# Kernel optimization log

Hardware: AMD Instinct MI355X
Metric: run time of the kernel (lower is better)

Reference implementation:

```python
import jax, jax.numpy as jnp
import numpy as np

D_MODEL = 768
D_STATE = 16
D_CONV = 4
EXPAND = 2
D_INNER = EXPAND * D_MODEL  # 1536
DT_RANK = -(-D_MODEL // 16)  # ceil(768/16) = 48
BATCH = 1
SEQ = 2048


def _silu(v):
    return v * jax.nn.sigmoid(v)


def setup_inputs() -> dict:
    key = jax.random.key(0)
    ks = jax.random.split(key, 8)
    s = 0.02
    x = jax.random.normal(ks[0], (BATCH, SEQ, D_MODEL), jnp.float32)
    in_proj_w = jax.random.normal(ks[1], (2 * D_INNER, D_MODEL), jnp.float32) * s
    conv_w = jax.random.normal(ks[2], (D_INNER, 1, D_CONV), jnp.float32) * s  # depthwise, groups=D_INNER
    conv_b = jnp.zeros((D_INNER,), jnp.float32)
    x_proj_w = jax.random.normal(ks[3], (DT_RANK + 2 * D_STATE, D_INNER), jnp.float32) * s
    dt_proj_w = jax.random.normal(ks[4], (D_INNER, DT_RANK), jnp.float32) * s
    dt_proj_b = jax.random.normal(ks[5], (D_INNER,), jnp.float32) * 0.01
    # A = repeat_interleave(arange(1, d_state+1), d_inner rows); A_log = log(A)
    A_log = jnp.log(jnp.tile(jnp.arange(1, D_STATE + 1, dtype=jnp.float32)[None, :], (D_INNER, 1)))
    D = jnp.ones((D_INNER,), jnp.float32)
    out_proj_w = jax.random.normal(ks[6], (D_MODEL, D_INNER), jnp.float32) * s
    return {"x": x, "in_proj_w": in_proj_w, "conv_w": conv_w, "conv_b": conv_b,
            "x_proj_w": x_proj_w, "dt_proj_w": dt_proj_w, "dt_proj_b": dt_proj_b,
            "A_log": A_log, "D": D, "out_proj_w": out_proj_w}


def reference(x, in_proj_w, conv_w, conv_b, x_proj_w, dt_proj_w, dt_proj_b, A_log, D, out_proj_w):
    b, L, d = x.shape
    # in_proj then split into x-branch and gate z
    xz = x @ in_proj_w.T                       # (b, L, 2*d_inner)
    xh, z = jnp.split(xz, 2, axis=-1)          # each (b, L, d_inner)
    # causal depthwise conv1d: torch pads d_conv-1 both sides then slices [:L];
    # equivalent to left-pad d_conv-1, right-pad 0
    xc = jnp.transpose(xh, (0, 2, 1))          # (b, d_inner, L)
    xc = jax.lax.conv_general_dilated(
        xc, conv_w, window_strides=(1,), padding=[(D_CONV - 1, 0)],
        feature_group_count=D_INNER, dimension_numbers=("NCH", "OIH", "NCH"))
    xc = xc + conv_b[None, :, None]
    u = _silu(jnp.transpose(xc, (0, 2, 1)))    # (b, L, d_inner)
    # input-dependent dt, B, C
    x_dbl = u @ x_proj_w.T                     # (b, L, dt_rank + 2*d_state)
    dt, Bm, Cm = jnp.split(x_dbl, [DT_RANK, DT_RANK + D_STATE], axis=-1)
    dt = jax.nn.softplus(dt @ dt_proj_w.T + dt_proj_b)  # (b, L, d_inner)
    A = -jnp.exp(A_log)                        # (d_inner, d_state)
    # selective scan via cumprod/cumsum (faithful to source math)
    dA = jnp.exp(dt[..., None] * A[None, None])              # (b, L, d_inner, d_state)
    dBu = dt[..., None] * Bm[:, :, None, :] * u[..., None]   # (b, L, d_inner, d_state)
    p = jnp.cumprod(dA, axis=1)
    eps = jnp.finfo(u.dtype).eps
    p_safe = jnp.maximum(p, eps)
    g = jnp.cumsum(dBu / p_safe, axis=1)
    h = g * p
    y = jnp.sum(h * Cm[:, :, None, :], axis=-1) + D * u      # (b, L, d_inner)
    y = y * _silu(z)
    return y @ out_proj_w.T                    # (b, L, d_model); dropout=identity (eval)
```

## Files before the change

### kernel.cpp

```cpp
#include <hip/hip_runtime.h>
#include <hip/hip_bf16.h>

#define LSEQ 2048
#define DMODEL 768
#define DINNER 1536
#define DSTATE 16
#define DTRANK 48
#define XDBL_W (DTRANK + 2*DSTATE)
#define CHUNK 64
#define NCHUNK (LSEQ / CHUNK)
#define NDN (DINNER * DSTATE)
#define FEPS 1.1920928955078125e-07f
#define SPLITK 8
#define OSPLIT 4
#define LDST 68

typedef short bf16x8 __attribute__((ext_vector_type(8)));
typedef float f32x4 __attribute__((ext_vector_type(4)));
typedef unsigned short u16;

__device__ __forceinline__ u16 f2bf_rn(float f) {
    unsigned u = __float_as_uint(f);
    unsigned r = u + 0x7FFFu + ((u >> 16) & 1u);
    return (u16)(r >> 16);
}
__device__ __forceinline__ float bf2f(u16 h) {
    return __uint_as_float(((unsigned)h) << 16);
}

__global__ __launch_bounds__(256) void cvt_split(
    const float* __restrict__ src, u16* __restrict__ hi, u16* __restrict__ lo, int n)
{
    int i = (blockIdx.x * 256 + threadIdx.x) * 4;
    if (i >= n) return;
    float4 v = *(const float4*)&src[i];
    u16 h0 = f2bf_rn(v.x), h1 = f2bf_rn(v.y), h2 = f2bf_rn(v.z), h3 = f2bf_rn(v.w);
    u16 l0 = f2bf_rn(v.x - bf2f(h0));
    u16 l1 = f2bf_rn(v.y - bf2f(h1));
    u16 l2 = f2bf_rn(v.z - bf2f(h2));
    u16 l3 = f2bf_rn(v.w - bf2f(h3));
    ushort4 hv = make_ushort4(h0, h1, h2, h3);
    ushort4 lv = make_ushort4(l0, l1, l2, l3);
    *(ushort4*)&hi[i] = hv;
    *(ushort4*)&lo[i] = lv;
}

__global__ __launch_bounds__(256) void mfma_gemm_tn(
    const u16* __restrict__ Ahi, const u16* __restrict__ Alo,
    const u16* __restrict__ Bhi, const u16* __restrict__ Blo,
    float* __restrict__ C, int ldc, int ldk, int Klen)
{
    __shared__ u16 lds[2 * 4 * 4096];
    const int tid = threadIdx.x;
    const int wid = tid >> 6;
    const int lane = tid & 63;
    const int m0 = blockIdx.x * 128;
    const int n0 = blockIdx.y * 128;
    const int Koff = blockIdx.z * Klen;

    const int st_subrow = lane >> 2;
    const int st_cphys = lane & 3;
    const u16* myplane = (wid == 0) ? Ahi : (wid == 1) ? Alo : (wid == 2) ? Bhi : Blo;
    const int rowbase = (wid < 2) ? m0 : n0;

    f32x4 acc[4][4] = {};
    const int wm = (wid >> 1) * 64;
    const int wn = (wid & 1) * 64;
    const int fr = lane & 15;
    const int fc = lane >> 4;
    const int nsteps = Klen / 32;

    auto stage = [&](int buf, int k0) {
#pragma unroll
        for (int j = 0; j < 8; ++j) {
            int row = j * 16 + st_subrow;
            int clog = st_cphys ^ ((row >> 1) & 3);
            const u16* g = myplane + (size_t)(rowbase + row) * ldk + k0 + clog * 8;
            u16* l = &lds[buf * 16384 + wid * 4096 + j * 512];
            __builtin_amdgcn_global_load_lds(
                (const __attribute__((address_space(1))) unsigned int*)g,
                (__attribute__((address_space(3))) unsigned int*)l, 16, 0, 0);
        }
    };

    stage(0, Koff);
    int cur = 0;
    for (int t = 0; t < nsteps; ++t) {
        __syncthreads();
        if (t + 1 < nsteps) stage(cur ^ 1, Koff + (t + 1) * 32);

        bf16x8 ah[4], al[4], bh[4], bl[4];
        const bf16x8* L = (const bf16x8*)&lds[cur * 16384];
#pragma unroll
        for (int mi = 0; mi < 4; ++mi) {
            int r = wm + mi * 16 + fr;
            int idx = r * 4 + (fc ^ ((r >> 1) & 3));
            ah[mi] = L[idx];
            al[mi] = L[512 + idx];
        }
#pragma unroll
        for (int nj = 0; nj < 4; ++nj) {
            int r = wn + nj * 16 + fr;
            int idx = r * 4 + (fc ^ ((r >> 1) & 3));
            bh[nj] = L[1024 + idx];
            bl[nj] = L[1536 + idx];
        }
#pragma unroll
        for (int mi = 0; mi < 4; ++mi)
#pragma unroll
            for (int nj = 0; nj < 4; ++nj) {
                acc[mi][nj] = __builtin_amdgcn_mfma_f32_16x16x32_bf16(ah[mi], bh[nj], acc[mi][nj], 0, 0, 0);
                acc[mi][nj] = __builtin_amdgcn_mfma_f32_16x16x32_bf16(ah[mi], bl[nj], acc[mi][nj], 0, 0, 0);
                acc[mi][nj] = __builtin_amdgcn_mfma_f32_16x16x32_bf16(al[mi], bh[nj], acc[mi][nj], 0, 0, 0);
            }
        cur ^= 1;
    }

    float* Cz = C + (size_t)blockIdx.z * LSEQ * ldc;
#pragma unroll
    for (int mi = 0; mi < 4; ++mi) {
        int row_b = m0 + wm + mi * 16 + (lane >> 4) * 4;
#pragma unroll
        for (int nj = 0; nj < 4; ++nj) {
            int col = n0 + wn + nj * 16 + (lane & 15);
#pragma unroll
            for (int r = 0; r < 4; ++r)
                Cz[(size_t)(row_b + r) * ldc + col] = acc[mi][nj][r];
        }
    }
}

__global__ __launch_bounds__(256) void reduce4(
    const float* __restrict__ Ppart, float* __restrict__ out, int n)
{
    int i = (blockIdx.x * 256 + threadIdx.x) * 4;
    if (i >= n) return;
    float4 a0 = *(const float4*)&Ppart[i];
    float4 a1 = *(const float4*)&Ppart[(size_t)n + i];
    float4 a2 = *(const float4*)&Ppart[(size_t)2 * n + i];
    float4 a3 = *(const float4*)&Ppart[(size_t)3 * n + i];
    float4 r;
    r.x = ((a0.x + a1.x) + a2.x) + a3.x;
    r.y = ((a0.y + a1.y) + a2.y) + a3.y;
    r.z = ((a0.z + a1.z) + a2.z) + a3.z;
    r.w = ((a0.w + a1.w) + a2.w) + a3.w;
    *(float4*)&out[i] = r;
}

template<int EPI>
__global__ __launch_bounds__(256) void gemm_tn(
    const float* __restrict__ A, int lda,
    const float* __restrict__ B, int ldb,
    float* __restrict__ C, int ldc,
    int M, int N, int K,
    const float* __restrict__ bias)
{
    __shared__ float As[16][64 + 4];
    __shared__ float Bs[16][64 + 4];
    const int tid = threadIdx.x;
    const int m0 = blockIdx.x * 64;
    const int n0 = blockIdx.y * 64;
    const int tx = tid & 15;
    const int ty = tid >> 4;
    const int lr = tid >> 4;
    const int lc = tid & 15;
    float acc[4][4] = {};

    for (int k0 = 0; k0 < K; k0 += 16) {
        const int k = k0 + lc;
#pragma unroll
        for (int i = 0; i < 4; ++i) {
            int m = m0 + lr + i * 16;
            As[lc][lr + i * 16] = (m < M) ? A[(size_t)m * lda + k] : 0.f;
        }
#pragma unroll
        for (int i = 0; i < 4; ++i) {
            int n = n0 + lr + i * 16;
            Bs[lc][lr + i * 16] = (n < N) ? B[(size_t)n * ldb + k] : 0.f;
        }
        __syncthreads();
#pragma unroll
        for (int kk = 0; kk < 16; ++kk) {
            float a[4], b[4];
#pragma unroll
            for (int i = 0; i < 4; ++i) a[i] = As[kk][ty * 4 + i];
#pragma unroll
            for (int j = 0; j < 4; ++j) b[j] = Bs[kk][tx * 4 + j];
#pragma unroll
            for (int i = 0; i < 4; ++i)
#pragma unroll
                for (int j = 0; j < 4; ++j)
                    acc[i][j] = fmaf(a[i], b[j], acc[i][j]);
        }
        __syncthreads();
    }

#pragma unroll
    for (int i = 0; i < 4; ++i) {
        int m = m0 + ty * 4 + i;
        if (m >= M) continue;
#pragma unroll
        for (int j = 0; j < 4; ++j) {
            int n = n0 + tx * 4 + j;
            if (n >= N) continue;
            float v = acc[i][j];
            if (EPI == 1) {
                v += bias[n];
                v = fmaxf(v, 0.f) + log1pf(expf(-fabsf(v)));
            }
            C[(size_t)m * ldc + n] = v;
        }
    }
}

__global__ __launch_bounds__(256) void gemm_tn_splitk(
    const float* __restrict__ A, int lda,
    const float* __restrict__ B, int ldb,
    float* __restrict__ Cpart, int ldc,
    int M, int N, int Kchunk)
{
    __shared__ float As[16][64 + 4];
    __shared__ float Bs[16][64 + 4];
    const int tid = threadIdx.x;
    const int m0 = blockIdx.x * 64;
    const int n0 = blockIdx.y * 64;
    const int kb = blockIdx.z * Kchunk;
    const int tx = tid & 15;
    const int ty = tid >> 4;
    const int lr = tid >> 4;
    const int lc = tid & 15;
    float acc[4][4] = {};

    for (int k0 = kb; k0 < kb + Kchunk; k0 += 16) {
        const int k = k0 + lc;
#pragma unroll
        for (int i = 0; i < 4; ++i) {
            int m = m0 + lr + i * 16;
            As[lc][lr + i * 16] = (m < M) ? A[(size_t)m * lda + k] : 0.f;
        }
#pragma unroll
        for (int i = 0; i < 4; ++i) {
            int n = n0 + lr + i * 16;
            Bs[lc][lr + i * 16] = (n < N) ? B[(size_t)n * ldb + k] : 0.f;
        }
        __syncthreads();
#pragma unroll
        for (int kk = 0; kk < 16; ++kk) {
            float a[4], b[4];
#pragma unroll
            for (int i = 0; i < 4; ++i) a[i] = As[kk][ty * 4 + i];
#pragma unroll
            for (int j = 0; j < 4; ++j) b[j] = Bs[kk][tx * 4 + j];
#pragma unroll
            for (int i = 0; i < 4; ++i)
#pragma unroll
                for (int j = 0; j < 4; ++j)
                    acc[i][j] = fmaf(a[i], b[j], acc[i][j]);
        }
        __syncthreads();
    }

    float* Cs = Cpart + (size_t)blockIdx.z * M * ldc;
#pragma unroll
    for (int i = 0; i < 4; ++i) {
        int m = m0 + ty * 4 + i;
        if (m >= M) continue;
#pragma unroll
        for (int j = 0; j < 4; ++j) {
            int n = n0 + tx * 4 + j;
            if (n >= N) continue;
            Cs[(size_t)m * ldc + n] = acc[i][j];
        }
    }
}

__global__ __launch_bounds__(256) void splitk_reduce(
    const float* __restrict__ Ppart, float* __restrict__ out, int n)
{
    int i = blockIdx.x * 256 + threadIdx.x;
    if (i >= n) return;
    float s = 0.f;
#pragma unroll
    for (int z = 0; z < SPLITK; ++z) s += Ppart[(size_t)z * n + i];
    out[i] = s;
}

__global__ __launch_bounds__(256) void conv_silu_kernel(
    const float* __restrict__ xz,
    const float* __restrict__ conv_w,
    const float* __restrict__ conv_b,
    float* __restrict__ u)
{
    int idx = blockIdx.x * blockDim.x + threadIdx.x;
    if (idx >= LSEQ * DINNER) return;
    int d = idx % DINNER;
    int t = idx / DINNER;
    float w[4];
#pragma unroll
    for (int j = 0; j < 4; ++j) w[j] = conv_w[d * 4 + j];
    float acc = conv_b[d];
#pragma unroll
    for (int j = 0; j < 4; ++j) {
        int s = t - 3 + j;
        if (s >= 0) acc = fmaf(xz[(size_t)s * (2 * DINNER) + d], w[j], acc);
    }
    float sig = 1.f / (1.f + __expf(-acc));
    u[idx] = acc * sig;
}

__global__ __launch_bounds__(256) void scan_chunkprod(
    const float* __restrict__ dtm,
    const float* __restrict__ A_log,
    float* __restrict__ P)
{
    __shared__ float sdtT[16][LDST];
    const int tid = threadIdx.x;
    const int d0 = blockIdx.x * 16;
    const int t0 = blockIdx.y * CHUNK;
    const int r = tid >> 4, c = tid & 15;
#pragma unroll
    for (int i = 0; i < 4; ++i) {
        int t = r + i * 16;
        sdtT[c][t] = dtm[(size_t)(t0 + t) * DINNER + d0 + c];
    }
    __syncthreads();
    const int n = tid & 15, dl = tid >> 4;
    const float Acoef = -expf(A_log[(d0 + dl) * DSTATE + n]);
    float s = 0.f;
#pragma unroll
    for (int tb = 0; tb < 16; ++tb) {
        f32x4 q = *(const f32x4*)&sdtT[dl][tb * 4];
        s += q[0] + q[1] + q[2] + q[3];
    }
    P[(size_t)blockIdx.y * NDN + d0 * DSTATE + tid] = __expf(Acoef * s);
}

template<int PROD>
__global__ __launch_bounds__(256) void scan_exclusive(float* __restrict__ buf)
{
    const int dn = blockIdx.x * 256 + threadIdx.x;
    float run = PROD ? 1.f : 0.f;
#pragma unroll
    for (int cidx = 0; cidx < NCHUNK; ++cidx) {
        float v = buf[(size_t)cidx * NDN + dn];
        buf[(size_t)cidx * NDN + dn] = run;
        run = PROD ? run * v : run + v;
    }
}

__global__ __launch_bounds__(256) void scan_chunksum(
    const float* __restrict__ dtm,
    const float* __restrict__ u,
    const float* __restrict__ xdbl,
    const float* __restrict__ A_log,
    const float* __restrict__ Ppre,
    float* __restrict__ S)
{
    __shared__ float sdtT[16][LDST], suT[16][LDST], sBT[16][LDST];
    const int tid = threadIdx.x;
    const int d0 = blockIdx.x * 16;
    const int t0 = blockIdx.y * CHUNK;
    const int r = tid >> 4, c = tid & 15;
#pragma unroll
    for (int i = 0; i < 4; ++i) {
        int t = r + i * 16;
        size_t row = (size_t)(t0 + t);
        sdtT[c][t] = dtm[row * DINNER + d0 + c];
        suT[c][t]  = u[row * DINNER + d0 + c];
        sBT[c][t]  = xdbl[row * XDBL_W + DTRANK + c];
    }
    __syncthreads();
    const int n = tid & 15, dl = tid >> 4;
    const float Acoef = -expf(A_log[(d0 + dl) * DSTATE + n]);
    float p = Ppre[(size_t)blockIdx.y * NDN + d0 * DSTATE + tid];
    float s = 0.f;
#pragma unroll
    for (int tb = 0; tb < 16; ++tb) {
        f32x4 dq = *(const f32x4*)&sdtT[dl][tb * 4];
        f32x4 uq = *(const f32x4*)&suT[dl][tb * 4];
        f32x4 bq = *(const f32x4*)&sBT[n][tb * 4];
#pragma unroll
        for (int j = 0; j < 4; ++j) {
            float dtv = dq[j];
            p *= __expf(dtv * Acoef);
            s += __fdividef((dtv * bq[j]) * uq[j], fmaxf(p, FEPS));
        }
    }
    S[(size_t)blockIdx.y * NDN + d0 * DSTATE + tid] = s;
}

__global__ __launch_bounds__(256) void scan_final(
    const float* __restrict__ dtm,
    const float* __restrict__ u,
    const float* __restrict__ xdbl,
    const float* __restrict__ A_log,
    const float* __restrict__ Ppre,
    const float* __restrict__ Gpre,
    float* __restrict__ xz)
{
    __shared__ float sdtT[16][LDST], suT[16][LDST], sBT[16][LDST], sCT[16][LDST];
    const int tid = threadIdx.x;
    const int d0 = blockIdx.x * 16;
    const int t0 = blockIdx.y * CHUNK;
    const int r = tid >> 4, c = tid & 15;
#pragma unroll
    for (int i = 0; i < 4; ++i) {
        int t = r + i * 16;
        size_t row = (size_t)(t0 + t);
        sdtT[c][t] = dtm[row * DINNER + d0 + c];
        suT[c][t]  = u[row * DINNER + d0 + c];
        sBT[c][t]  = xdbl[row * XDBL_W + DTRANK + c];
        sCT[c][t]  = xdbl[row * XDBL_W + DTRANK + DSTATE + c];
    }
    __syncthreads();
    const int n = tid & 15, dl = tid >> 4;
    const int d = d0 + dl;
    const float Acoef = -expf(A_log[d * DSTATE + n]);
    float p = Ppre[(size_t)blockIdx.y * NDN + d0 * DSTATE + tid];
    float g = Gpre[(size_t)blockIdx.y * NDN + d0 * DSTATE + tid];
#pragma unroll
    for (int tb = 0; tb < 16; ++tb) {
        f32x4 dq = *(const f32x4*)&sdtT[dl][tb * 4];
        f32x4 uq = *(const f32x4*)&suT[dl][tb * 4];
        f32x4 bq = *(const f32x4*)&sBT[n][tb * 4];
        f32x4 cq = *(const f32x4*)&sCT[n][tb * 4];
#pragma unroll
        for (int j = 0; j < 4; ++j) {
            float dtv = dq[j];
            p *= __expf(dtv * Acoef);
            g += __fdividef((dtv * bq[j]) * uq[j], fmaxf(p, FEPS));
            float part = (g * p) * cq[j];
            part += __shfl_xor(part, 1, 16);
            part += __shfl_xor(part, 2, 16);
            part += __shfl_xor(part, 4, 16);
            part += __shfl_xor(part, 8, 16);
            if (n == 0)
                xz[(size_t)(t0 + tb * 4 + j) * (2 * DINNER) + d] = part;
        }
    }
}

__global__ __launch_bounds__(256) void gate_kernel(
    const float* __restrict__ xz,
    const float* __restrict__ u,
    const float* __restrict__ Dvec,
    u16* __restrict__ yhi, u16* __restrict__ ylo)
{
    int i4 = (blockIdx.x * 256 + threadIdx.x) * 4;
    if (i4 >= LSEQ * DINNER) return;
    int t = i4 / DINNER;
    int d = i4 - t * DINNER;
    size_t base = (size_t)t * (2 * DINNER) + d;
    float4 part = *(const float4*)&xz[base];
    float4 zv   = *(const float4*)&xz[base + DINNER];
    float4 uv   = *(const float4*)&u[i4];
    float4 Dd   = *(const float4*)&Dvec[d];
    float pa[4] = {part.x, part.y, part.z, part.w};
    float za[4] = {zv.x, zv.y, zv.z, zv.w};
    float ua[4] = {uv.x, uv.y, uv.z, uv.w};
    float Da[4] = {Dd.x, Dd.y, Dd.z, Dd.w};
    u16 ha[4], la[4];
#pragma unroll
    for (int j = 0; j < 4; ++j) {
        float sig = 1.f / (1.f + __expf(-za[j]));
        float yv = (pa[j] + Da[j] * ua[j]) * (za[j] * sig);
        ha[j] = f2bf_rn(yv);
        la[j] = f2bf_rn(yv - bf2f(ha[j]));
    }
    *(ushort4*)&yhi[i4] = make_ushort4(ha[0], ha[1], ha[2], ha[3]);
    *(ushort4*)&ylo[i4] = make_ushort4(la[0], la[1], la[2], la[3]);
}

extern "C" void kernel_launch(void* const* d_in, const int* in_sizes, int n_in,
                              void* d_out, int out_size, void* d_ws, size_t ws_size,
                              hipStream_t stream) {
    const float* x          = (const float*)d_in[0];
    const float* in_proj_w  = (const float*)d_in[1];
    const float* conv_w     = (const float*)d_in[2];
    const float* conv_b     = (const float*)d_in[3];
    const float* x_proj_w   = (const float*)d_in[4];
    const float* dt_proj_w  = (const float*)d_in[5];
    const float* dt_proj_b  = (const float*)d_in[6];
    const float* A_log      = (const float*)d_in[7];
    const float* Dvec       = (const float*)d_in[8];
    const float* out_proj_w = (const float*)d_in[9];
    float* out = (float*)d_out;

    char* w = (char*)d_ws;
    auto alloc = [&](size_t bytes) { char* p = w; w += (bytes + 255) & ~(size_t)255; return p; };

    float* xz    = (float*)alloc((size_t)LSEQ * 2 * DINNER * 4);
    float* u     = (float*)alloc((size_t)LSEQ * DINNER * 4);
    float* xdbl  = (float*)alloc((size_t)LSEQ * XDBL_W * 4);
    float* dtb   = (float*)alloc((size_t)LSEQ * DINNER * 4);
    float* P     = (float*)alloc((size_t)NCHUNK * NDN * 4);
    float* S     = (float*)alloc((size_t)NCHUNK * NDN * 4);
    float* Ppart = (float*)alloc((size_t)SPLITK * LSEQ * XDBL_W * 4);
    u16* xhi  = (u16*)alloc((size_t)LSEQ * DMODEL * 2);
    u16* xlo  = (u16*)alloc((size_t)LSEQ * DMODEL * 2);
    u16* wihi = (u16*)alloc((size_t)2 * DINNER * DMODEL * 2);
    u16* wilo = (u16*)alloc((size_t)2 * DINNER * DMODEL * 2);
    u16* owhi = (u16*)alloc((size_t)DMODEL * DINNER * 2);
    u16* owlo = (u16*)alloc((size_t)DMODEL * DINNER * 2);
    u16* yhi  = (u16*)alloc((size_t)LSEQ * DINNER * 2);
    u16* ylo  = (u16*)alloc((size_t)LSEQ * DINNER * 2);
    float* opart = u;

    dim3 blk(256);

    cvt_split<<<(LSEQ * DMODEL) / 1024, blk, 0, stream>>>(x, xhi, xlo, LSEQ * DMODEL);
    cvt_split<<<(2 * DINNER * DMODEL) / 1024, blk, 0, stream>>>(in_proj_w, wihi, wilo, 2 * DINNER * DMODEL);
    cvt_split<<<(DMODEL * DINNER) / 1024, blk, 0, stream>>>(out_proj_w, owhi, owlo, DMODEL * DINNER);

    mfma_gemm_tn<<<dim3(LSEQ / 128, (2 * DINNER) / 128, 1), blk, 0, stream>>>(
        xhi, xlo, wihi, wilo, xz, 2 * DINNER, DMODEL, DMODEL);

    conv_silu_kernel<<<(LSEQ * DINNER + 255) / 256, blk, 0, stream>>>(xz, conv_w, conv_b, u);

    gemm_tn_splitk<<<dim3(LSEQ / 64, (XDBL_W + 63) / 64, SPLITK), blk, 0, stream>>>(
        u, DINNER, x_proj_w, DINNER, Ppart, XDBL_W, LSEQ, XDBL_W, DINNER / SPLITK);
    splitk_reduce<<<(LSEQ * XDBL_W + 255) / 256, blk, 0, stream>>>(Ppart, xdbl, LSEQ * XDBL_W);

    gemm_tn<1><<<dim3(LSEQ / 64, DINNER / 64), blk, 0, stream>>>(
        xdbl, XDBL_W, dt_proj_w, DTRANK, dtb, DINNER, LSEQ, DINNER, DTRANK, dt_proj_b);

    scan_chunkprod<<<dim3(DINNER / 16, NCHUNK), blk, 0, stream>>>(dtb, A_log, P);
    scan_exclusive<1><<<NDN / 256, blk, 0, stream>>>(P);
    scan_chunksum<<<dim3(DINNER / 16, NCHUNK), blk, 0, stream>>>(dtb, u, xdbl, A_log, P, S);
    scan_exclusive<0><<<NDN / 256, blk, 0, stream>>>(S);
    scan_final<<<dim3(DINNER / 16, NCHUNK), blk, 0, stream>>>(
        dtb, u, xdbl, A_log, P, S, xz);

    gate_kernel<<<(LSEQ * DINNER) / 1024, blk, 0, stream>>>(xz, u, Dvec, yhi, ylo);

    mfma_gemm_tn<<<dim3(LSEQ / 128, DMODEL / 128, OSPLIT), blk, 0, stream>>>(
        yhi, ylo, owhi, owlo, opart, DMODEL, DINNER, DINNER / OSPLIT);
    reduce4<<<(LSEQ * DMODEL) / 1024, blk, 0, stream>>>(opart, out, LSEQ * DMODEL);
}
```

Before: 243.8 us.

## Give each scan_final thread four states and reduce with DPP quad permutes

scan_final now handles 64 channels per block instead of 16. Each thread owns four state indices of one channel, so the per-timestep reduction over 16 states becomes in-thread FMAs plus two DPP quad-permute adds, replacing four cross-lane shuffles. Loads of dt and u into LDS are amortized over more channels, and the B/C tiles are reused across four times as many channels. The grid shrinks fourfold and register use per thread grows, which may reduce occupancy and latency hiding.

```diff
diff --git a/kernel.cpp b/kernel.cpp
--- a/kernel.cpp
+++ b/kernel.cpp
@@ -28,6 +28,12 @@
     return __uint_as_float(((unsigned)h) << 16);
 }
 
+template<int CTRL>
+__device__ __forceinline__ float qperm(float x) {
+    return __int_as_float(__builtin_amdgcn_update_dpp(
+        0, __float_as_int(x), CTRL, 0xF, 0xF, true));
+}
+
 __global__ __launch_bounds__(256) void cvt_split(
     const float* __restrict__ src, u16* __restrict__ hi, u16* __restrict__ lo, int n)
 {
@@ -39,10 +45,8 @@
     u16 l1 = f2bf_rn(v.y - bf2f(h1));
     u16 l2 = f2bf_rn(v.z - bf2f(h2));
     u16 l3 = f2bf_rn(v.w - bf2f(h3));
-    ushort4 hv = make_ushort4(h0, h1, h2, h3);
-    ushort4 lv = make_ushort4(l0, l1, l2, l3);
-    *(ushort4*)&hi[i] = hv;
-    *(ushort4*)&lo[i] = lv;
+    *(ushort4*)&hi[i] = make_ushort4(h0, h1, h2, h3);
+    *(ushort4*)&lo[i] = make_ushort4(l0, l1, l2, l3);
 }
 
 __global__ __launch_bounds__(256) void mfma_gemm_tn(
@@ -398,43 +402,71 @@
     const float* __restrict__ Gpre,
     float* __restrict__ xz)
 {
-    __shared__ float sdtT[16][LDST], suT[16][LDST], sBT[16][LDST], sCT[16][LDST];
+    __shared__ float sdtT[64][LDST], suT[64][LDST];
+    __shared__ float sBT[16][LDST], sCT[16][LDST];
     const int tid = threadIdx.x;
-    const int d0 = blockIdx.x * 16;
+    const int d0 = blockIdx.x * 64;
     const int t0 = blockIdx.y * CHUNK;
-    const int r = tid >> 4, c = tid & 15;
+
+#pragma unroll
+    for (int i = 0; i < 16; ++i) {
+        int idx = i * 256 + tid;
+        int dl = idx & 63, t = idx >> 6;
+        size_t row = (size_t)(t0 + t);
+        sdtT[dl][t] = dtm[row * DINNER + d0 + dl];
+        suT[dl][t]  = u[row * DINNER + d0 + dl];
+    }
 #pragma unroll
     for (int i = 0; i < 4; ++i) {
-        int t = r + i * 16;
+        int idx = i * 256 + tid;
+        int n = idx & 15, t = idx >> 4;
         size_t row = (size_t)(t0 + t);
-        sdtT[c][t] = dtm[row * DINNER + d0 + c];
-        suT[c][t]  = u[row * DINNER + d0 + c];
-        sBT[c][t]  = xdbl[row * XDBL_W + DTRANK + c];
-        sCT[c][t]  = xdbl[row * XDBL_W + DTRANK + DSTATE + c];
+        sBT[n][t] = xdbl[row * XDBL_W + DTRANK + n];
+        sCT[n][t] = xdbl[row * XDBL_W + DTRANK + DSTATE + n];
     }
     __syncthreads();
-    const int n = tid & 15, dl = tid >> 4;
-    const int d = d0 + dl;
-    const float Acoef = -expf(A_log[d * DSTATE + n]);
-    float p = Ppre[(size_t)blockIdx.y * NDN + d0 * DSTATE + tid];
-    float g = Gpre[(size_t)blockIdx.y * NDN + d0 * DSTATE + tid];
+
+    const int lane = tid & 63, wid = tid >> 6;
+    const int dloc = wid * 16 + (lane >> 2);
+    const int d = d0 + dloc;
+    const int nq = lane & 3;
+
+    f32x4 Ar = *(const f32x4*)&A_log[d * DSTATE + nq * 4];
+    float Ac[4] = {-expf(Ar[0]), -expf(Ar[1]), -expf(Ar[2]), -expf(Ar[3])};
+    size_t pgbase = (size_t)blockIdx.y * NDN + (size_t)d * DSTATE + nq * 4;
+    f32x4 p = *(const f32x4*)&Ppre[pgbase];
+    f32x4 g = *(const f32x4*)&Gpre[pgbase];
+
 #pragma unroll
     for (int tb = 0; tb < 16; ++tb) {
-        f32x4 dq = *(const f32x4*)&sdtT[dl][tb * 4];
-        f32x4 uq = *(const f32x4*)&suT[dl][tb * 4];
-        f32x4 bq = *(const f32x4*)&sBT[n][tb * 4];
-        f32x4 cq = *(const f32x4*)&sCT[n][tb * 4];
+        f32x4 dq = *(const f32x4*)&sdtT[dloc][tb * 4];
+        f32x4 uq = *(const f32x4*)&suT[dloc][tb * 4];
+        f32x4 b0 = *(const f32x4*)&sBT[nq * 4 + 0][tb * 4];
+        f32x4 b1 = *(const f32x4*)&sBT[nq * 4 + 1][tb * 4];
+        f32x4 b2 = *(const f32x4*)&sBT[nq * 4 + 2][tb * 4];
+        f32x4 b3 = *(const f32x4*)&sBT[nq * 4 + 3][tb * 4];
+        f32x4 c0 = *(const f32x4*)&sCT[nq * 4 + 0][tb * 4];
+        f32x4 c1 = *(const f32x4*)&sCT[nq * 4 + 1][tb * 4];
+        f32x4 c2 = *(const f32x4*)&sCT[nq * 4 + 2][tb * 4];
+        f32x4 c3 = *(const f32x4*)&sCT[nq * 4 + 3][tb * 4];
 #pragma unroll
         for (int j = 0; j < 4; ++j) {
-            float dtv = dq[j];
-            p *= __expf(dtv * Acoef);
-            g += __fdividef((dtv * bq[j]) * uq[j], fmaxf(p, FEPS));
-            float part = (g * p) * cq[j];
-            part += __shfl_xor(part, 1, 16);
-            part += __shfl_xor(part, 2, 16);
-            part += __shfl_xor(part, 4, 16);
-            part += __shfl_xor(part, 8, 16);
-            if (n == 0)
+            float dtv = dq[j], uv = uq[j];
+            p[0] *= __expf(dtv * Ac[0]);
+            p[1] *= __expf(dtv * Ac[1]);
+            p[2] *= __expf(dtv * Ac[2]);
+            p[3] *= __expf(dtv * Ac[3]);
+            g[0] += __fdividef((dtv * b0[j]) * uv, fmaxf(p[0], FEPS));
+            g[1] += __fdividef((dtv * b1[j]) * uv, fmaxf(p[1], FEPS));
+            g[2] += __fdividef((dtv * b2[j]) * uv, fmaxf(p[2], FEPS));
+            g[3] += __fdividef((dtv * b3[j]) * uv, fmaxf(p[3], FEPS));
+            float part = (g[0] * p[0]) * c0[j];
+            part = fmaf(g[1] * p[1], c1[j], part);
+            part = fmaf(g[2] * p[2], c2[j], part);
+            part = fmaf(g[3] * p[3], c3[j], part);
+            part += qperm<0xB1>(part);
+            part += qperm<0x4E>(part);
+            if (nq == 0)
                 xz[(size_t)(t0 + tb * 4 + j) * (2 * DINNER) + d] = part;
         }
     }
@@ -528,7 +560,7 @@
     scan_exclusive<1><<<NDN / 256, blk, 0, stream>>>(P);
     scan_chunksum<<<dim3(DINNER / 16, NCHUNK), blk, 0, stream>>>(dtb, u, xdbl, A_log, P, S);
     scan_exclusive<0><<<NDN / 256, blk, 0, stream>>>(S);
-    scan_final<<<dim3(DINNER / 16, NCHUNK), blk, 0, stream>>>(
+    scan_final<<<dim3(DINNER / 64, NCHUNK), blk, 0, stream>>>(
         dtb, u, xdbl, A_log, P, S, xz);
 
     gate_kernel<<<(LSEQ * DINNER) / 1024, blk, 0, stream>>>(xz, u, Dvec, yhi, ylo);
```

Measured after the change: 238.2 us. 2.3% less time.
